# Kernel optimization log

Hardware: AMD Instinct MI355X
Metric: run time of the kernel (lower is better)

## Reference

```python
import jax, jax.numpy as jnp
import numpy as np

N_TILES, NX = 6, 96
IN_C, HID_C = 128, 256
BATCH = 4


def _build_neighbors(n_tiles=N_TILES, nx=NX):
    # 4-connectivity on each tile with periodic wrap (fixed cubed-sphere-style
    # grid graph; preserves the gather/mean access pattern of build_dgl_graph).
    i, j = np.meshgrid(np.arange(nx), np.arange(nx), indexing='ij')
    idx = lambda ii, jj: (ii % nx) * nx + (jj % nx)
    per_tile = np.stack([idx(i - 1, j), idx(i + 1, j), idx(i, j - 1), idx(i, j + 1)],
                        axis=-1).reshape(nx * nx, 4)
    offsets = (np.arange(n_tiles) * nx * nx)[:, None, None]
    return (per_tile[None] + offsets).reshape(-1, 4).astype(np.int32)


def setup_inputs() -> dict:
    key = jax.random.key(0)
    ks = jax.random.split(key, 6)
    s = lambda fan_in: 1.0 / np.sqrt(fan_in)
    return {
        'x': jax.random.normal(ks[0], (BATCH, N_TILES, NX, NX, IN_C), jnp.float32),
        'neighbors': jnp.asarray(_build_neighbors()),
        'W_self1': jax.random.normal(ks[1], (IN_C, HID_C), jnp.float32) * s(IN_C),
        'W_neigh1': jax.random.normal(ks[2], (IN_C, HID_C), jnp.float32) * s(IN_C),
        'b1': jnp.zeros((HID_C,), jnp.float32),
        'W_self2': jax.random.normal(ks[3], (HID_C, HID_C), jnp.float32) * s(HID_C),
        'W_neigh2': jax.random.normal(ks[4], (HID_C, HID_C), jnp.float32) * s(HID_C),
        'b2': jnp.zeros((HID_C,), jnp.float32),
    }


def _sage_conv(h, neighbors, W_self, W_neigh, b):
    # h: [B, N, C]; neighbors: [N, 4] -> mean-aggregated SAGEConv
    h_neigh = jnp.mean(h[:, neighbors], axis=2)  # [B, N, 4, C] -> [B, N, C]
    return jnp.einsum('bnc,cd->bnd', h, W_self) + \
           jnp.einsum('bnc,cd->bnd', h_neigh, W_neigh) + b


def reference(x, neighbors, W_self1, W_neigh1, b1, W_self2, W_neigh2, b2):
    B, T, X, Y, C = x.shape
    h = x.reshape(B, T * X * Y, C)                      # flatten sphere -> nodes
    h = jax.nn.relu(_sage_conv(h, neighbors, W_self1, W_neigh1, b1))
    h = jax.nn.relu(_sage_conv(h, neighbors, W_self2, W_neigh2, b2))
    return h.reshape(B, T, X, Y, -1)
```

## Files before the change

### kernel.cpp

```cpp
#include <hip/hip_runtime.h>
#include <stdint.h>

typedef __attribute__((ext_vector_type(8))) short short8;
typedef __attribute__((ext_vector_type(4))) float f32x4;

#define NNODES 55296
#define DOUT 256

#define WAIT_VM(N) asm volatile("s_waitcnt vmcnt(" #N ")" ::: "memory")
#define SOFT_FENCE asm volatile("" ::: "memory")

__device__ __forceinline__ float bf2f(unsigned short h) {
    union { unsigned u; float f; } x; x.u = ((unsigned)h) << 16; return x.f;
}
__device__ __forceinline__ unsigned short f2bf(float f) {
    union { float f; unsigned u; } x; x.f = f;
    return (unsigned short)((x.u + 0x7fffu + ((x.u >> 16) & 1u)) >> 16);
}

__device__ __forceinline__ void storev(float* p, float v) { *p = v; }
__device__ __forceinline__ void storev(unsigned short* p, float v) { *p = f2bf(v); }

__device__ __forceinline__ void dma16(const void* g, void* l) {
    __builtin_amdgcn_global_load_lds(
        reinterpret_cast<const unsigned int __attribute__((address_space(1)))*>((uintptr_t)g),
        reinterpret_cast<unsigned int __attribute__((address_space(3)))*>((uintptr_t)l),
        16, 0, 0);
}

__device__ __forceinline__ short8 frag_self(const float* p) {
    float4 a = *(const float4*)p, b = *(const float4*)(p + 4);
    union { short8 s; unsigned short u[8]; } r;
    r.u[0] = f2bf(a.x); r.u[1] = f2bf(a.y); r.u[2] = f2bf(a.z); r.u[3] = f2bf(a.w);
    r.u[4] = f2bf(b.x); r.u[5] = f2bf(b.y); r.u[6] = f2bf(b.z); r.u[7] = f2bf(b.w);
    return r.s;
}
__device__ __forceinline__ short8 frag_self(const unsigned short* p) {
    return *(const short8*)p;
}
__device__ __forceinline__ void acc8(const float* p, float* o) {
    float4 a = *(const float4*)p, b = *(const float4*)(p + 4);
    o[0] += a.x; o[1] += a.y; o[2] += a.z; o[3] += a.w;
    o[4] += b.x; o[5] += b.y; o[6] += b.z; o[7] += b.w;
}
__device__ __forceinline__ void acc8(const unsigned short* p, float* o) {
    uint4 v = *(const uint4*)p;
    const unsigned short* u = (const unsigned short*)&v;
#pragma unroll
    for (int i = 0; i < 8; ++i) o[i] += bf2f(u[i]);
}
template <typename TIN>
__device__ __forceinline__ short8 frag_mean4(const TIN* p0, const TIN* p1,
                                             const TIN* p2, const TIN* p3) {
    float s[8] = {0.f, 0.f, 0.f, 0.f, 0.f, 0.f, 0.f, 0.f};
    acc8(p0, s); acc8(p1, s); acc8(p2, s); acc8(p3, s);
    union { short8 s8; unsigned short u[8]; } r;
#pragma unroll
    for (int i = 0; i < 8; ++i) r.u[i] = f2bf(s[i] * 0.25f);
    return r.s8;
}

__global__ void build_wt(const float* __restrict__ Ws,
                         const float* __restrict__ Wn,
                         unsigned short* __restrict__ Wt, int C) {
    int K2 = 2 * C;
    int idx = blockIdx.x * 256 + threadIdx.x;
    if (idx >= 256 * K2) return;
    int d = idx / K2;
    int k = idx - d * K2;
    float v = (k < C) ? Ws[(size_t)k * DOUT + d] : Wn[(size_t)(k - C) * DOUT + d];
    Wt[idx] = f2bf(v);
}

template <int C, typename TIN>
__global__ __launch_bounds__(256) void mean_pass(const TIN* __restrict__ hin,
                                                 const int* __restrict__ nbr,
                                                 unsigned short* __restrict__ hm) {
    constexpr int CPL = C / 8;
    const int idx = blockIdx.x * 256 + threadIdx.x;
    const int node = idx / CPL;
    const int ch = (idx - node * CPL) * 8;
    const int b = node / NNODES;
    const int n = node - b * NNODES;
    const size_t bbase = (size_t)b * NNODES;
    const int4 nb = *(const int4*)(nbr + (size_t)n * 4);
    float s[8] = {0.f, 0.f, 0.f, 0.f, 0.f, 0.f, 0.f, 0.f};
    acc8(hin + (bbase + nb.x) * (size_t)C + ch, s);
    acc8(hin + (bbase + nb.y) * (size_t)C + ch, s);
    acc8(hin + (bbase + nb.z) * (size_t)C + ch, s);
    acc8(hin + (bbase + nb.w) * (size_t)C + ch, s);
    union { uint4 v; unsigned short u[8]; } r;
#pragma unroll
    for (int i = 0; i < 8; ++i) r.u[i] = f2bf(s[i] * 0.25f);
    *(uint4*)(hm + (size_t)node * C + ch) = r.v;
}

__global__ __launch_bounds__(512) void sage_v7_l2(
    const unsigned short* __restrict__ h1p,
    const unsigned short* __restrict__ hmp,
    const unsigned short* __restrict__ Wt,
    const float* __restrict__ bias,
    float* __restrict__ out) {
    extern __shared__ char lds[];
    const int tid = threadIdx.x;
    const int bid = blockIdx.x;
    const int yg = bid & 1;
    const int rb = bid >> 1;
    const int gcol0 = yg * 128;
    const int rowbase = rb * 256;

    const int l = tid & 63;
    const int w = tid >> 6;
    const int lr = l & 15, lg = l >> 4;
    const int rowg = w >> 1;
    const int colb = (w & 1) * 64;

    const char* wsrc = (const char*)Wt + (size_t)gcol0 * 1024;

    auto stageW = [&](int s) {
#pragma unroll
        for (int i = 0; i < 8; ++i) {
            int o = (tid + i * 512) * 16;
            int col = o >> 9, kb = o & 511;
            uint4 v = *(const uint4*)(wsrc + (size_t)col * 1024 + s * 512 + kb);
            *(uint4*)(lds + (o ^ ((col & 7) << 4))) = v;
        }
    };

    auto issueA = [&](int p) {
        const char* base = (p < 8) ? (const char*)h1p : (const char*)hmp;
        const int kb = (p & 7) * 64;
        char* ldst = lds + 65536 + (p & 3) * 16384 + w * 1024;
#pragma unroll
        for (int i = 0; i < 2; ++i) {
            int c = tid + i * 512;
            int row = c >> 2, slot = c & 3;
            const char* src = base + (size_t)(rowbase + row) * 512 + kb +
                              ((slot ^ (row & 3)) << 4);
            dma16(src, ldst + i * 8192);
        }
    };

    issueA(0); issueA(1); issueA(2);
    stageW(0);
    __syncthreads();

    f32x4 acc[4][4];
#pragma unroll
    for (int m = 0; m < 4; ++m)
#pragma unroll
        for (int j = 0; j < 4; ++j) acc[m][j] = (f32x4){0.f, 0.f, 0.f, 0.f};

    int arow0[4];
#pragma unroll
    for (int m = 0; m < 4; ++m) arow0[m] = rowg * 64 + m * 16 + lr;

#pragma unroll
    for (int kk = 0; kk < 16; ++kk) {
        if (kk <= 13) { WAIT_VM(4); }
        else if (kk == 14) { WAIT_VM(2); }
        else { WAIT_VM(0); }
        __builtin_amdgcn_s_barrier();
        SOFT_FENCE;
        if (kk == 8) {
            stageW(1);
            __syncthreads();
        }
        if (kk + 3 < 16) issueA(kk + 3);

        const int bufo = 65536 + (kk & 3) * 16384;
        short8 af[4], wf[4];
#pragma unroll
        for (int m = 0; m < 4; ++m) {
            const int ar = arow0[m];
            af[m] = *(const short8*)(lds + bufo + ar * 64 + ((lg ^ (ar & 3)) << 4));
        }
#pragma unroll
        for (int j = 0; j < 4; ++j) {
            const int col = colb + j * 16 + lr;
            wf[j] = *(const short8*)(
                lds + (((col << 9) + ((kk & 7) << 6) + (lg << 4)) ^ ((lr & 7) << 4)));
        }
#pragma unroll
        for (int j = 0; j < 4; ++j)
#pragma unroll
            for (int m = 0; m < 4; ++m)
                acc[m][j] = __builtin_amdgcn_mfma_f32_16x16x32_bf16(af[m], wf[j], acc[m][j], 0, 0, 0);
        SOFT_FENCE;
    }

#pragma unroll
    for (int j = 0; j < 4; ++j) {
        const int gcol = gcol0 + colb + j * 16 + lr;
        const float bv = bias[gcol];
#pragma unroll
        for (int m = 0; m < 4; ++m) {
#pragma unroll
            for (int r = 0; r < 4; ++r) {
                const int row = rowbase + rowg * 64 + m * 16 + lg * 4 + r;
                out[(size_t)row * DOUT + gcol] = fmaxf(acc[m][j][r] + bv, 0.f);
            }
        }
    }
}

template <int C, typename TIN, typename TOUT>
__global__ __launch_bounds__(512, 2) void sage_v5(
    const TIN* __restrict__ hin, const unsigned short* __restrict__ hm,
    const unsigned short* __restrict__ Wt, const float* __restrict__ bias,
    TOUT* __restrict__ out) {
    constexpr int K2 = 2 * C;
    constexpr int ROWB = K2 * 2;
    constexpr int LCOLS = 131072 / ROWB;
    constexpr int CG = LCOLS / 64;
    constexpr int RG = 8 / CG;
    constexpr int CGRID = 256 / LCOLS;
    constexpr int NK = K2 / 32;
    constexpr int D = (sizeof(TIN) == 4) ? 3 : 4;
    extern __shared__ char Bs[];

    const int tid = threadIdx.x;
    const int bid = blockIdx.x;
    const int yg = bid % CGRID;
    const int rb = bid / CGRID;
    const int gcol0 = yg * LCOLS;

    {
        const char* src = (const char*)(Wt + (size_t)gcol0 * K2);
#pragma unroll
        for (int i = 0; i < 16; ++i) {
            int byt = (i * 512 + tid) * 16;
            uint4 v = *(const uint4*)(src + byt);
            int c = byt / ROWB;
            *(uint4*)(Bs + (byt ^ ((c & 7) << 4))) = v;
        }
    }
    __syncthreads();

    const int l = tid & 63;
    const int w = tid >> 6;
    const int rowg = w / CG;
    const int colb = (w % CG) * 64;
    const int lr = l & 15, lg = l >> 4;

    const int rowbase = rb * (RG * 64) + rowg * 64;
    const char* hb = (const char*)hin;
    const char* hmb = (const char*)hm;

    unsigned sofs[4], mofs[4];
#pragma unroll
    for (int m = 0; m < 4; ++m) {
        const int r = rowbase + m * 16 + lr;
        sofs[m] = (unsigned)(((size_t)r * C + lg * 8) * sizeof(TIN));
        mofs[m] = (unsigned)(((size_t)r * C + lg * 8) * 2);
    }

    f32x4 acc[4][4];
#pragma unroll
    for (int m = 0; m < 4; ++m)
#pragma unroll
        for (int j = 0; j < 4; ++j) acc[m][j] = (f32x4){0.f, 0.f, 0.f, 0.f};

    auto loadA = [&](int kk, short8* a) {
        const int k0 = kk * 32;
        if (k0 < C) {
#pragma unroll
            for (int m = 0; m < 4; ++m)
                a[m] = frag_self((const TIN*)(hb + sofs[m] + (unsigned)k0 * sizeof(TIN)));
        } else {
#pragma unroll
            for (int m = 0; m < 4; ++m)
                a[m] = *(const short8*)(hmb + mofs[m] + (unsigned)(k0 - C) * 2);
        }
    };

    short8 ab[D][4];
#pragma unroll
    for (int p = 0; p < D; ++p) loadA(p, ab[p]);

#pragma unroll
    for (int kk = 0; kk < NK; ++kk) {
        const int k0 = kk * 32;
        short8 cur[4];
#pragma unroll
        for (int m = 0; m < 4; ++m) cur[m] = ab[kk % D][m];
        if (kk + D < NK) loadA(kk + D, ab[kk % D]);
#pragma unroll
        for (int j = 0; j < 4; ++j) {
            const int c = colb + j * 16 + lr;
            const short8 bf = *(const short8*)(
                Bs + ((c * ROWB + (k0 + lg * 8) * 2) ^ ((l & 7) << 4)));
#pragma unroll
            for (int m = 0; m < 4; ++m)
                acc[m][j] = __builtin_amdgcn_mfma_f32_16x16x32_bf16(cur[m], bf, acc[m][j], 0, 0, 0);
        }
    }

#pragma unroll
    for (int j = 0; j < 4; ++j) {
        const int gcol = gcol0 + colb + j * 16 + lr;
        const float bv = bias[gcol];
#pragma unroll
        for (int m = 0; m < 4; ++m) {
#pragma unroll
            for (int r = 0; r < 4; ++r) {
                const int row = rowbase + m * 16 + lg * 4 + r;
                storev(out + (size_t)row * DOUT + gcol, fmaxf(acc[m][j][r] + bv, 0.f));
            }
        }
    }
}

template <int C, typename TIN, typename TOUT>
__global__ __launch_bounds__(512, 2) void sage_v3(
    const TIN* __restrict__ hin, const int* __restrict__ nbr,
    const unsigned short* __restrict__ Wt, const float* __restrict__ bias,
    TOUT* __restrict__ out) {
    constexpr int K2 = 2 * C;
    constexpr int ROWB = K2 * 2;
    constexpr int LCOLS = 131072 / ROWB;
    constexpr int CG = LCOLS / 128;
    constexpr int RG = 8 / CG;
    extern __shared__ char Bs[];

    const int tid = threadIdx.x;
    const int gcol0 = blockIdx.y * LCOLS;
    {
        const char* src = (const char*)(Wt + (size_t)gcol0 * K2);
#pragma unroll
        for (int i = 0; i < 16; ++i) {
            int byt = (i * 512 + tid) * 16;
            uint4 v = *(const uint4*)(src + byt);
            int c = byt / ROWB;
            *(uint4*)(Bs + (byt ^ ((c & 7) << 4))) = v;
        }
    }
    __syncthreads();

    const int l = tid & 63;
    const int w = tid >> 6;
    const int rowg = w / CG;
    const int colb = (w % CG) * 128;
    const int lr = l & 15, lg = l >> 4;

    const int rowbase = blockIdx.x * (RG * 64) + rowg * 64;
    const int bb = rowbase / NNODES;
    const int n0 = rowbase - bb * NNODES;
    const size_t bbase = (size_t)bb * NNODES;

    unsigned soff[4], noff[4][4];
#pragma unroll
    for (int m = 0; m < 4; ++m) {
        int r = m * 16 + lr;
        soff[m] = (unsigned)(((rowbase + r) * (size_t)C + lg * 8) * sizeof(TIN));
        int4 nb = *(const int4*)(nbr + (size_t)(n0 + r) * 4);
        noff[m][0] = (unsigned)(((bbase + nb.x) * C + lg * 8) * sizeof(TIN));
        noff[m][1] = (unsigned)(((bbase + nb.y) * C + lg * 8) * sizeof(TIN));
        noff[m][2] = (unsigned)(((bbase + nb.z) * C + lg * 8) * sizeof(TIN));
        noff[m][3] = (unsigned)(((bbase + nb.w) * C + lg * 8) * sizeof(TIN));
    }
    const char* hb = (const char*)hin;

    f32x4 acc[4][8];
#pragma unroll
    for (int m = 0; m < 4; ++m)
#pragma unroll
        for (int j = 0; j < 8; ++j) acc[m][j] = (f32x4){0.f, 0.f, 0.f, 0.f};

#pragma unroll
    for (int kk = 0; kk < K2 / 32; ++kk) {
        const int k0 = kk * 32;
        short8 a[4];
        if (k0 < C) {
            const unsigned kb = k0 * sizeof(TIN);
#pragma unroll
            for (int m = 0; m < 4; ++m)
                a[m] = frag_self((const TIN*)(hb + soff[m] + kb));
        } else {
            const unsigned kb = (k0 - C) * sizeof(TIN);
#pragma unroll
            for (int m = 0; m < 4; ++m)
                a[m] = frag_mean4((const TIN*)(hb + noff[m][0] + kb),
                                  (const TIN*)(hb + noff[m][1] + kb),
                                  (const TIN*)(hb + noff[m][2] + kb),
                                  (const TIN*)(hb + noff[m][3] + kb));
        }
#pragma unroll
        for (int j = 0; j < 8; ++j) {
            const int c = colb + j * 16 + lr;
            const short8 bf = *(const short8*)(
                Bs + ((c * ROWB + (k0 + lg * 8) * 2) ^ ((l & 7) << 4)));
#pragma unroll
            for (int m = 0; m < 4; ++m)
                acc[m][j] = __builtin_amdgcn_mfma_f32_16x16x32_bf16(a[m], bf, acc[m][j], 0, 0, 0);
        }
    }

#pragma unroll
    for (int j = 0; j < 8; ++j) {
        const int gcol = gcol0 + colb + j * 16 + lr;
        const float bv = bias[gcol];
#pragma unroll
        for (int m = 0; m < 4; ++m) {
#pragma unroll
            for (int r = 0; r < 4; ++r) {
                const int row = rowbase + m * 16 + lg * 4 + r;
                storev(out + (size_t)row * DOUT + gcol, fmaxf(acc[m][j][r] + bv, 0.f));
            }
        }
    }
}

extern "C" void kernel_launch(void* const* d_in, const int* in_sizes, int n_in,
                              void* d_out, int out_size, void* d_ws, size_t ws_size,
                              hipStream_t stream) {
    const float* x = (const float*)d_in[0];
    const int* nbr = (const int*)d_in[1];
    const float* Ws1 = (const float*)d_in[2];
    const float* Wn1 = (const float*)d_in[3];
    const float* b1 = (const float*)d_in[4];
    const float* Ws2 = (const float*)d_in[5];
    const float* Wn2 = (const float*)d_in[6];
    const float* b2 = (const float*)d_in[7];
    float* out = (float*)d_out;

    const int B = in_sizes[0] / (NNODES * 128);
    const int M = B * NNODES;

    char* ws = (char*)d_ws;
    const size_t h1_bytes = (size_t)M * DOUT * 2;
    const size_t hm_bytes = (size_t)M * DOUT * 2;
    const size_t need = h1_bytes + hm_bytes + 131072 + 262144;

    if (ws_size >= need) {
        unsigned short* h1 = (unsigned short*)ws;
        unsigned short* hm = (unsigned short*)(ws + h1_bytes);
        unsigned short* Wt1 = (unsigned short*)(ws + h1_bytes + hm_bytes);
        unsigned short* Wt2 = Wt1 + 256 * 256;

        build_wt<<<256, 256, 0, stream>>>(Ws1, Wn1, Wt1, 128);
        build_wt<<<512, 256, 0, stream>>>(Ws2, Wn2, Wt2, 256);

        hipFuncSetAttribute((const void*)sage_v5<128, float, unsigned short>,
                            hipFuncAttributeMaxDynamicSharedMemorySize, 131072);
        hipFuncSetAttribute((const void*)sage_v7_l2,
                            hipFuncAttributeMaxDynamicSharedMemorySize, 131072);

        mean_pass<128, float><<<M * 16 / 256, 256, 0, stream>>>(x, nbr, hm);
        sage_v5<128, float, unsigned short>
            <<<M / 128, 512, 131072, stream>>>(x, hm, Wt1, b1, h1);
        mean_pass<256, unsigned short><<<M * 32 / 256, 256, 0, stream>>>(h1, nbr, hm);
        sage_v7_l2<<<(M / 256) * 2, 512, 131072, stream>>>(h1, hm, Wt2, b2, out);
    } else {
        unsigned short* h1 = (unsigned short*)ws;
        unsigned short* Wt1 = (unsigned short*)(ws + h1_bytes);
        unsigned short* Wt2 = Wt1 + 256 * 256;

        build_wt<<<256, 256, 0, stream>>>(Ws1, Wn1, Wt1, 128);
        build_wt<<<512, 256, 0, stream>>>(Ws2, Wn2, Wt2, 256);

        hipFuncSetAttribute((const void*)sage_v3<128, float, unsigned short>,
                            hipFuncAttributeMaxDynamicSharedMemorySize, 131072);
        hipFuncSetAttribute((const void*)sage_v3<256, unsigned short, float>,
                            hipFuncAttributeMaxDynamicSharedMemorySize, 131072);

        sage_v3<128, float, unsigned short>
            <<<dim3(M / 256, 1), 512, 131072, stream>>>(x, nbr, Wt1, b1, h1);
        sage_v3<256, unsigned short, float>
            <<<dim3(M / 512, 2), 512, 131072, stream>>>(h1, nbr, Wt2, b2, out);
    }
}
```

Baseline: 362.3 us.

## Pre-pack bf16 self+mean layer-1 input and use LDS-DMA pipelined GEMM

Layer 1 now starts with a kernel that converts x to bf16 and writes it, together with the neighbor mean, into one concatenated [M,256] bf16 buffer. A new layer-1 GEMM kernel streams that buffer into LDS through async global_load_lds with a multi-stage pipeline and stages the weights in two halves, computing all 256 output columns per block. Both GEMMs swap MFMA operand order so each lane holds four consecutive columns, which allows vectorized bias loads and packed stores. The cost is an extra write and read of the bf16 self copy of x in exchange for halving the GEMM's fp32 input reads and overlapping loads with MFMA work.

```diff
diff --git a/kernel.cpp b/kernel.cpp
--- a/kernel.cpp
+++ b/kernel.cpp
@@ -70,6 +70,32 @@
     int k = idx - d * K2;
     float v = (k < C) ? Ws[(size_t)k * DOUT + d] : Wn[(size_t)(k - C) * DOUT + d];
     Wt[idx] = f2bf(v);
+}
+
+__global__ __launch_bounds__(256) void mean_xb(const float* __restrict__ x,
+                                               const int* __restrict__ nbr,
+                                               unsigned short* __restrict__ xm) {
+    const int idx = blockIdx.x * 256 + threadIdx.x;
+    const int node = idx >> 4;
+    const int ch = (idx & 15) * 8;
+    const int b = node / NNODES;
+    const int n = node - b * NNODES;
+    const size_t bbase = (size_t)b * NNODES;
+    const int4 nb = *(const int4*)(nbr + (size_t)n * 4);
+    const float* ps = x + (size_t)node * 128 + ch;
+    union { uint4 v; unsigned short u[8]; } rs, rm;
+    float4 a0 = *(const float4*)ps, a1 = *(const float4*)(ps + 4);
+    rs.u[0] = f2bf(a0.x); rs.u[1] = f2bf(a0.y); rs.u[2] = f2bf(a0.z); rs.u[3] = f2bf(a0.w);
+    rs.u[4] = f2bf(a1.x); rs.u[5] = f2bf(a1.y); rs.u[6] = f2bf(a1.z); rs.u[7] = f2bf(a1.w);
+    float s[8] = {0.f, 0.f, 0.f, 0.f, 0.f, 0.f, 0.f, 0.f};
+    acc8(x + (bbase + nb.x) * 128 + ch, s);
+    acc8(x + (bbase + nb.y) * 128 + ch, s);
+    acc8(x + (bbase + nb.z) * 128 + ch, s);
+    acc8(x + (bbase + nb.w) * 128 + ch, s);
+#pragma unroll
+    for (int i = 0; i < 8; ++i) rm.u[i] = f2bf(s[i] * 0.25f);
+    *(uint4*)(xm + (size_t)node * 256 + ch) = rs.v;
+    *(uint4*)(xm + (size_t)node * 256 + 128 + ch) = rm.v;
 }
 
 template <int C, typename TIN>
@@ -95,7 +121,107 @@
     *(uint4*)(hm + (size_t)node * C + ch) = r.v;
 }
 
-__global__ __launch_bounds__(512) void sage_v7_l2(
+__global__ __launch_bounds__(512) void sage_v8_l1(
+    const unsigned short* __restrict__ xm,
+    const unsigned short* __restrict__ Wt,
+    const float* __restrict__ bias,
+    unsigned short* __restrict__ out) {
+    extern __shared__ char lds[];
+    const int tid = threadIdx.x;
+    const int rowbase = blockIdx.x * 256;
+    const int l = tid & 63, w = tid >> 6;
+    const int lr = l & 15, lg = l >> 4;
+    const int rowg = w >> 1;
+    const int colb = (w & 1) * 128;
+    const char* wsrc = (const char*)Wt;
+    const char* xb = (const char*)xm;
+
+    auto stageW = [&](int s) {
+#pragma unroll
+        for (int i = 0; i < 8; ++i) {
+            int o = (tid + i * 512) * 16;
+            int col = o >> 8, kb = o & 255;
+            uint4 v = *(const uint4*)(wsrc + (size_t)col * 512 + s * 256 + kb);
+            *(uint4*)(lds + (o ^ ((col & 7) << 4))) = v;
+        }
+    };
+    auto issueA = [&](int p) {
+        const int kb = p * 64;
+        char* ldst = lds + 65536 + (p & 3) * 16384 + w * 1024;
+#pragma unroll
+        for (int i = 0; i < 2; ++i) {
+            int c = tid + i * 512;
+            int row = c >> 2, slot = c & 3;
+            const char* src = xb + (size_t)(rowbase + row) * 512 + kb +
+                              ((slot ^ (row & 3)) << 4);
+            dma16(src, ldst + i * 8192);
+        }
+    };
+
+    issueA(0); issueA(1); issueA(2);
+    stageW(0);
+    __syncthreads();
+
+    f32x4 acc[4][8];
+#pragma unroll
+    for (int m = 0; m < 4; ++m)
+#pragma unroll
+        for (int j = 0; j < 8; ++j) acc[m][j] = (f32x4){0.f, 0.f, 0.f, 0.f};
+
+    int arow0[4];
+#pragma unroll
+    for (int m = 0; m < 4; ++m) arow0[m] = rowg * 64 + m * 16 + lr;
+
+#pragma unroll
+    for (int kk = 0; kk < 8; ++kk) {
+        if (kk <= 5) { WAIT_VM(4); }
+        else if (kk == 6) { WAIT_VM(2); }
+        else { WAIT_VM(0); }
+        __builtin_amdgcn_s_barrier();
+        SOFT_FENCE;
+        if (kk == 4) {
+            stageW(1);
+            __syncthreads();
+        }
+        if (kk + 3 < 8) issueA(kk + 3);
+
+        const int bufo = 65536 + (kk & 3) * 16384;
+        short8 af[4];
+#pragma unroll
+        for (int m = 0; m < 4; ++m) {
+            const int ar = arow0[m];
+            af[m] = *(const short8*)(lds + bufo + ar * 64 + ((lg ^ (ar & 3)) << 4));
+        }
+#pragma unroll
+        for (int j = 0; j < 8; ++j) {
+            const int col = colb + j * 16 + lr;
+            const short8 wf = *(const short8*)(
+                lds + ((col * 256 + (kk & 3) * 64 + lg * 16) ^ ((col & 7) << 4)));
+#pragma unroll
+            for (int m = 0; m < 4; ++m)
+                acc[m][j] = __builtin_amdgcn_mfma_f32_16x16x32_bf16(wf, af[m], acc[m][j], 0, 0, 0);
+        }
+        SOFT_FENCE;
+    }
+
+#pragma unroll
+    for (int m = 0; m < 4; ++m) {
+        const int row = rowbase + rowg * 64 + m * 16 + lr;
+#pragma unroll
+        for (int j = 0; j < 8; ++j) {
+            const int c0 = colb + j * 16 + lg * 4;
+            const float4 bv = *(const float4*)(bias + c0);
+            union { unsigned short u[4]; uint2 v; } pk;
+            pk.u[0] = f2bf(fmaxf(acc[m][j][0] + bv.x, 0.f));
+            pk.u[1] = f2bf(fmaxf(acc[m][j][1] + bv.y, 0.f));
+            pk.u[2] = f2bf(fmaxf(acc[m][j][2] + bv.z, 0.f));
+            pk.u[3] = f2bf(fmaxf(acc[m][j][3] + bv.w, 0.f));
+            *(uint2*)(out + (size_t)row * 256 + c0) = pk.v;
+        }
+    }
+}
+
+__global__ __launch_bounds__(512) void sage_v8_l2(
     const unsigned short* __restrict__ h1p,
     const unsigned short* __restrict__ hmp,
     const unsigned short* __restrict__ Wt,
@@ -185,128 +311,23 @@
         for (int j = 0; j < 4; ++j)
 #pragma unroll
             for (int m = 0; m < 4; ++m)
-                acc[m][j] = __builtin_amdgcn_mfma_f32_16x16x32_bf16(af[m], wf[j], acc[m][j], 0, 0, 0);
+                acc[m][j] = __builtin_amdgcn_mfma_f32_16x16x32_bf16(wf[j], af[m], acc[m][j], 0, 0, 0);
         SOFT_FENCE;
     }
 
 #pragma unroll
-    for (int j = 0; j < 4; ++j) {
-        const int gcol = gcol0 + colb + j * 16 + lr;
-        const float bv = bias[gcol];
-#pragma unroll
-        for (int m = 0; m < 4; ++m) {
-#pragma unroll
-            for (int r = 0; r < 4; ++r) {
-                const int row = rowbase + rowg * 64 + m * 16 + lg * 4 + r;
-                out[(size_t)row * DOUT + gcol] = fmaxf(acc[m][j][r] + bv, 0.f);
-            }
-        }
-    }
-}
-
-template <int C, typename TIN, typename TOUT>
-__global__ __launch_bounds__(512, 2) void sage_v5(
-    const TIN* __restrict__ hin, const unsigned short* __restrict__ hm,
-    const unsigned short* __restrict__ Wt, const float* __restrict__ bias,
-    TOUT* __restrict__ out) {
-    constexpr int K2 = 2 * C;
-    constexpr int ROWB = K2 * 2;
-    constexpr int LCOLS = 131072 / ROWB;
-    constexpr int CG = LCOLS / 64;
-    constexpr int RG = 8 / CG;
-    constexpr int CGRID = 256 / LCOLS;
-    constexpr int NK = K2 / 32;
-    constexpr int D = (sizeof(TIN) == 4) ? 3 : 4;
-    extern __shared__ char Bs[];
-
-    const int tid = threadIdx.x;
-    const int bid = blockIdx.x;
-    const int yg = bid % CGRID;
-    const int rb = bid / CGRID;
-    const int gcol0 = yg * LCOLS;
-
-    {
-        const char* src = (const char*)(Wt + (size_t)gcol0 * K2);
-#pragma unroll
-        for (int i = 0; i < 16; ++i) {
-            int byt = (i * 512 + tid) * 16;
-            uint4 v = *(const uint4*)(src + byt);
-            int c = byt / ROWB;
-            *(uint4*)(Bs + (byt ^ ((c & 7) << 4))) = v;
-        }
-    }
-    __syncthreads();
-
-    const int l = tid & 63;
-    const int w = tid >> 6;
-    const int rowg = w / CG;
-    const int colb = (w % CG) * 64;
-    const int lr = l & 15, lg = l >> 4;
-
-    const int rowbase = rb * (RG * 64) + rowg * 64;
-    const char* hb = (const char*)hin;
-    const char* hmb = (const char*)hm;
-
-    unsigned sofs[4], mofs[4];
-#pragma unroll
     for (int m = 0; m < 4; ++m) {
-        const int r = rowbase + m * 16 + lr;
-        sofs[m] = (unsigned)(((size_t)r * C + lg * 8) * sizeof(TIN));
-        mofs[m] = (unsigned)(((size_t)r * C + lg * 8) * 2);
-    }
-
-    f32x4 acc[4][4];
-#pragma unroll
-    for (int m = 0; m < 4; ++m)
-#pragma unroll
-        for (int j = 0; j < 4; ++j) acc[m][j] = (f32x4){0.f, 0.f, 0.f, 0.f};
-
-    auto loadA = [&](int kk, short8* a) {
-        const int k0 = kk * 32;
-        if (k0 < C) {
-#pragma unroll
-            for (int m = 0; m < 4; ++m)
-                a[m] = frag_self((const TIN*)(hb + sofs[m] + (unsigned)k0 * sizeof(TIN)));
-        } else {
-#pragma unroll
-            for (int m = 0; m < 4; ++m)
-                a[m] = *(const short8*)(hmb + mofs[m] + (unsigned)(k0 - C) * 2);
-        }
-    };
-
-    short8 ab[D][4];
-#pragma unroll
-    for (int p = 0; p < D; ++p) loadA(p, ab[p]);
-
-#pragma unroll
-    for (int kk = 0; kk < NK; ++kk) {
-        const int k0 = kk * 32;
-        short8 cur[4];
-#pragma unroll
-        for (int m = 0; m < 4; ++m) cur[m] = ab[kk % D][m];
-        if (kk + D < NK) loadA(kk + D, ab[kk % D]);
+        const int row = rowbase + rowg * 64 + m * 16 + lr;
 #pragma unroll
         for (int j = 0; j < 4; ++j) {
-            const int c = colb + j * 16 + lr;
-            const short8 bf = *(const short8*)(
-                Bs + ((c * ROWB + (k0 + lg * 8) * 2) ^ ((l & 7) << 4)));
-#pragma unroll
-            for (int m = 0; m < 4; ++m)
-                acc[m][j] = __builtin_amdgcn_mfma_f32_16x16x32_bf16(cur[m], bf, acc[m][j], 0, 0, 0);
-        }
-    }
-
-#pragma unroll
-    for (int j = 0; j < 4; ++j) {
-        const int gcol = gcol0 + colb + j * 16 + lr;
-        const float bv = bias[gcol];
-#pragma unroll
-        for (int m = 0; m < 4; ++m) {
-#pragma unroll
-            for (int r = 0; r < 4; ++r) {
-                const int row = rowbase + m * 16 + lg * 4 + r;
-                storev(out + (size_t)row * DOUT + gcol, fmaxf(acc[m][j][r] + bv, 0.f));
-            }
+            const int gcol = gcol0 + colb + j * 16 + lg * 4;
+            const float4 bv = *(const float4*)(bias + gcol);
+            float4 o;
+            o.x = fmaxf(acc[m][j][0] + bv.x, 0.f);
+            o.y = fmaxf(acc[m][j][1] + bv.y, 0.f);
+            o.z = fmaxf(acc[m][j][2] + bv.z, 0.f);
+            o.w = fmaxf(acc[m][j][3] + bv.w, 0.f);
+            *(float4*)(out + (size_t)row * 256 + gcol) = o;
         }
     }
 }
@@ -434,23 +455,22 @@
 
     if (ws_size >= need) {
         unsigned short* h1 = (unsigned short*)ws;
-        unsigned short* hm = (unsigned short*)(ws + h1_bytes);
+        unsigned short* xm = (unsigned short*)(ws + h1_bytes);
         unsigned short* Wt1 = (unsigned short*)(ws + h1_bytes + hm_bytes);
         unsigned short* Wt2 = Wt1 + 256 * 256;
 
         build_wt<<<256, 256, 0, stream>>>(Ws1, Wn1, Wt1, 128);
         build_wt<<<512, 256, 0, stream>>>(Ws2, Wn2, Wt2, 256);
 
-        hipFuncSetAttribute((const void*)sage_v5<128, float, unsigned short>,
+        hipFuncSetAttribute((const void*)sage_v8_l1,
                             hipFuncAttributeMaxDynamicSharedMemorySize, 131072);
-        hipFuncSetAttribute((const void*)sage_v7_l2,
+        hipFuncSetAttribute((const void*)sage_v8_l2,
                             hipFuncAttributeMaxDynamicSharedMemorySize, 131072);
 
-        mean_pass<128, float><<<M * 16 / 256, 256, 0, stream>>>(x, nbr, hm);
-        sage_v5<128, float, unsigned short>
-            <<<M / 128, 512, 131072, stream>>>(x, hm, Wt1, b1, h1);
-        mean_pass<256, unsigned short><<<M * 32 / 256, 256, 0, stream>>>(h1, nbr, hm);
-        sage_v7_l2<<<(M / 256) * 2, 512, 131072, stream>>>(h1, hm, Wt2, b2, out);
+        mean_xb<<<M / 16, 256, 0, stream>>>(x, nbr, xm);
+        sage_v8_l1<<<M / 256, 512, 131072, stream>>>(xm, Wt1, b1, h1);
+        mean_pass<256, unsigned short><<<M * 32 / 256, 256, 0, stream>>>(h1, nbr, xm);
+        sage_v8_l2<<<(M / 256) * 2, 512, 131072, stream>>>(h1, xm, Wt2, b2, out);
     } else {
         unsigned short* h1 = (unsigned short*)ws;
         unsigned short* Wt1 = (unsigned short*)(ws + h1_bytes);
```

Result: faster. 345.7 us (-4.6%).
